# Kernel tuning notes

Hardware: AMD Instinct MI355X
Metric: run time of the kernel (lower is better)

## Reference

```python
import jax, jax.numpy as jnp
import numpy as np

N_ATOMS = 64
NC2 = N_ATOMS * (N_ATOMS - 1) // 2  # 2016
BATCH = 1024


def _pair_mask(n_atoms):
    """mask[i, p] = 1 if atom i is a member of pair p.

    Pair enumeration matches the original code: for i2 in range(n_atoms),
    for j2 in range(i2) -> row-major lower-triangle order, which is exactly
    np.tril_indices(n_atoms, k=-1).
    """
    i2, j2 = np.tril_indices(n_atoms, k=-1)
    nc2 = i2.shape[0]
    mask = np.zeros((n_atoms, nc2), dtype=np.float32)
    p = np.arange(nc2)
    mask[i2, p] = 1.0
    mask[j2, p] = 1.0
    return jnp.asarray(mask)


_MASK = _pair_mask(N_ATOMS)  # [n_atoms, NC2]


def setup_inputs() -> dict:
    key = jax.random.key(0)
    _NRF = jax.random.normal(key, (BATCH, NC2), dtype=jnp.float32)
    return {"_NRF": _NRF}


def reference(_NRF):
    # Original: Triangle unpacks flat NC2 -> symmetric [N,N] (zero diag),
    # divides by 2, then for each atom i scatters tri_NRF[:, i, partner]
    # into pair slot p iff i is in pair p. Net effect:
    #   eij_NRF[b, i, p] = _NRF[b, p] / 2  if atom i in pair p else 0
    # [B, n_atoms, NC2]
    return _MASK[None, :, :] * (_NRF[:, None, :] * 0.5)
```

## Files before the change

### kernel.cpp

```cpp
#include <hip/hip_runtime.h>


typedef float f32x4 __attribute__((ext_vector_type(4)));

__device__ __forceinline__ int pair_row(int p) {
    float f = sqrtf(8.0f * (float)p + 1.0f);
    int i = (int)((1.0f + f) * 0.5f);
    while (i * (i - 1) / 2 > p) --i;
    while ((i + 1) * i / 2 <= p) ++i;
    return i;
}

__global__ __launch_bounds__(256) void transform_nrf_kernel(
    const float* __restrict__ nrf, float* __restrict__ out) {
    const int t     = blockIdx.x * 256 + threadIdx.x;
    const int pos   = t % 32256;
    const int slice = t / 32256;
    const int i     = pos / 504;
    const int p4    = pos % 504;
    const int p0    = p4 * 4;

    bool m[4];
#pragma unroll
    for (int k = 0; k < 4; ++k) {
        const int p  = p0 + k;
        const int r  = pair_row(p);
        const int j  = p - r * (r - 1) / 2;
        m[k] = (i == r) || (i == j);
    }

    const f32x4* __restrict__ nrf4 = (const f32x4*)nrf;
    f32x4* __restrict__ out4       = (f32x4*)out;

    const int bbase = slice * 64;
#pragma unroll 8
    for (int k = 0; k < 64; ++k) {
        const int b = bbase + k;
        const f32x4 v = nrf4[b * 504 + p4];
        f32x4 o;
        o.x = m[0] ? v.x * 0.5f : 0.0f;
        o.y = m[1] ? v.y * 0.5f : 0.0f;
        o.z = m[2] ? v.z * 0.5f : 0.0f;
        o.w = m[3] ? v.w * 0.5f : 0.0f;
        __builtin_nontemporal_store(o, &out4[(size_t)(b * 64 + i) * 504 + p4]);
    }
}

extern "C" void kernel_launch(void* const* d_in, const int* in_sizes, int n_in,
                              void* d_out, int out_size, void* d_ws, size_t ws_size,
                              hipStream_t stream) {
    const float* nrf = (const float*)d_in[0];
    float* out       = (float*)d_out;
    transform_nrf_kernel<<<2016, 256, 0, stream>>>(nrf, out);
}
```

Before: 98.61 us.

## Remap threads to load each input vector once and write 16 atom rows

Each thread now handles one batch row and one pair-quad, loading the input vector once and emitting 16 consecutive atom rows. Previously each thread covered one atom row across 64 batch rows, reloading input per row. The grid grows fourfold, and the pair-index decode now runs per batch row. Membership tests are done per atom row inside the unrolled loop.

```diff
diff --git a/kernel.cpp b/kernel.cpp
--- a/kernel.cpp
+++ b/kernel.cpp
@@ -13,36 +13,40 @@
 
 __global__ __launch_bounds__(256) void transform_nrf_kernel(
     const float* __restrict__ nrf, float* __restrict__ out) {
-    const int t     = blockIdx.x * 256 + threadIdx.x;
-    const int pos   = t % 32256;
-    const int slice = t / 32256;
-    const int i     = pos / 504;
-    const int p4    = pos % 504;
-    const int p0    = p4 * 4;
+    const int t  = blockIdx.x * 256 + threadIdx.x;
+    const int p4 = t % 504;
+    const int r1 = t / 504;
+    const int b  = r1 % 1024;
+    const int iq = r1 / 1024;
+    const int p0 = p4 * 4;
 
-    bool m[4];
+    int ia[4], jb[4];
 #pragma unroll
     for (int k = 0; k < 4; ++k) {
-        const int p  = p0 + k;
-        const int r  = pair_row(p);
-        const int j  = p - r * (r - 1) / 2;
-        m[k] = (i == r) || (i == j);
+        const int p = p0 + k;
+        const int r = pair_row(p);
+        ia[k] = r;
+        jb[k] = p - r * (r - 1) / 2;
     }
 
-    const f32x4* __restrict__ nrf4 = (const f32x4*)nrf;
-    f32x4* __restrict__ out4       = (f32x4*)out;
+    const f32x4 v = ((const f32x4*)nrf)[b * 504 + p4];
+    f32x4 val;
+    val.x = v.x * 0.5f; val.y = v.y * 0.5f;
+    val.z = v.z * 0.5f; val.w = v.w * 0.5f;
 
-    const int bbase = slice * 64;
-#pragma unroll 8
-    for (int k = 0; k < 64; ++k) {
-        const int b = bbase + k;
-        const f32x4 v = nrf4[b * 504 + p4];
+    f32x4* __restrict__ out4 = (f32x4*)out;
+    const int i0   = iq * 16;
+    const int base = (b * 64 + i0) * 504 + p4;
+
+#pragma unroll
+    for (int k = 0; k < 16; ++k) {
+        const int i = i0 + k;
         f32x4 o;
-        o.x = m[0] ? v.x * 0.5f : 0.0f;
-        o.y = m[1] ? v.y * 0.5f : 0.0f;
-        o.z = m[2] ? v.z * 0.5f : 0.0f;
-        o.w = m[3] ? v.w * 0.5f : 0.0f;
-        __builtin_nontemporal_store(o, &out4[(size_t)(b * 64 + i) * 504 + p4]);
+        o.x = (i == ia[0] || i == jb[0]) ? val.x : 0.0f;
+        o.y = (i == ia[1] || i == jb[1]) ? val.y : 0.0f;
+        o.z = (i == ia[2] || i == jb[2]) ? val.z : 0.0f;
+        o.w = (i == ia[3] || i == jb[3]) ? val.w : 0.0f;
+        __builtin_nontemporal_store(o, &out4[base + k * 504]);
     }
 }
 
@@ -51,5 +55,5 @@
                               hipStream_t stream) {
     const float* nrf = (const float*)d_in[0];
     float* out       = (float*)d_out;
-    transform_nrf_kernel<<<2016, 256, 0, stream>>>(nrf, out);
+    transform_nrf_kernel<<<8064, 256, 0, stream>>>(nrf, out);
 }
```

Measured after the change: 101.6 us. 1.03x slower.

## Flatten output indexing: each wave writes contiguous float4 chunks, recompute mask per element

Applied to the files above, without the earlier changes.

Replaces the per-thread loop over 64 batch rows with a flat mapping in which each wave writes four consecutive 64-float4 chunks of the output. The grid grows to 32256 blocks. Stores become fully contiguous across lanes, in place of one row per thread striding across batch. The pair mask is now recomputed per element, with an incremental row update replacing three of the four sqrt-based searches. This adds ALU work and many more blocks, and each input float4 is reloaded per atom row, relying on cache.

```diff
diff --git a/kernel.cpp b/kernel.cpp
--- a/kernel.cpp
+++ b/kernel.cpp
@@ -13,36 +13,37 @@
 
 __global__ __launch_bounds__(256) void transform_nrf_kernel(
     const float* __restrict__ nrf, float* __restrict__ out) {
-    const int t     = blockIdx.x * 256 + threadIdx.x;
-    const int pos   = t % 32256;
-    const int slice = t / 32256;
-    const int i     = pos / 504;
-    const int p4    = pos % 504;
-    const int p0    = p4 * 4;
-
-    bool m[4];
-#pragma unroll
-    for (int k = 0; k < 4; ++k) {
-        const int p  = p0 + k;
-        const int r  = pair_row(p);
-        const int j  = p - r * (r - 1) / 2;
-        m[k] = (i == r) || (i == j);
-    }
+    const unsigned wid   = threadIdx.x >> 6;
+    const unsigned lane  = threadIdx.x & 63u;
+    const unsigned wbase = blockIdx.x * 1024u + wid * 256u;
 
     const f32x4* __restrict__ nrf4 = (const f32x4*)nrf;
     f32x4* __restrict__ out4       = (f32x4*)out;
 
-    const int bbase = slice * 64;
-#pragma unroll 8
-    for (int k = 0; k < 64; ++k) {
-        const int b = bbase + k;
-        const f32x4 v = nrf4[b * 504 + p4];
-        f32x4 o;
-        o.x = m[0] ? v.x * 0.5f : 0.0f;
-        o.y = m[1] ? v.y * 0.5f : 0.0f;
-        o.z = m[2] ? v.z * 0.5f : 0.0f;
-        o.w = m[3] ? v.w * 0.5f : 0.0f;
-        __builtin_nontemporal_store(o, &out4[(size_t)(b * 64 + i) * 504 + p4]);
+#pragma unroll
+    for (int jj = 0; jj < 4; ++jj) {
+        const unsigned f   = wbase + jj * 64u + lane;
+        const unsigned row = f / 504u;
+        const unsigned p4  = f - row * 504u;
+        const unsigned b   = row >> 6;
+        const int      i   = (int)(row & 63u);
+        const int      p0  = (int)(p4 * 4u);
+
+        const f32x4 v = nrf4[b * 504u + p4];
+        const float vv[4] = {v.x * 0.5f, v.y * 0.5f, v.z * 0.5f, v.w * 0.5f};
+
+        int t = pair_row(p0);
+        float oo[4];
+#pragma unroll
+        for (int c = 0; c < 4; ++c) {
+            const int p = p0 + c;
+            if (c > 0) t += (p >= ((t + 1) * t) / 2) ? 1 : 0;
+            const int j2 = p - (t * (t - 1)) / 2;
+            oo[c] = ((i == t) || (i == j2)) ? vv[c] : 0.0f;
+        }
+
+        f32x4 o = {oo[0], oo[1], oo[2], oo[3]};
+        __builtin_nontemporal_store(o, &out4[f]);
     }
 }
 
@@ -51,5 +52,5 @@
                               hipStream_t stream) {
     const float* nrf = (const float*)d_in[0];
     float* out       = (float*)d_out;
-    transform_nrf_kernel<<<2016, 256, 0, stream>>>(nrf, out);
+    transform_nrf_kernel<<<32256, 256, 0, stream>>>(nrf, out);
 }
```

New measurement: 85.54 us. 13.3% less time.
